# Kernel optimization log

Measured on AMD Instinct MI355X. Metric: run time of the kernel, lower is better.

## Reference

```python
import jax, jax.numpy as jnp
import numpy as np

UNITS = 1024
FT_DIM = 512
TIME_HORIZON = 512
INVERT_INDEX = 64
BATCH = 64


def setup_inputs() -> dict:
    key = jax.random.key(0)
    k1, k2, k3 = jax.random.split(key, 3)
    inputs = jax.random.normal(k1, (BATCH, TIME_HORIZON, FT_DIM), dtype=jnp.float32)
    # R ~ RandomNormal(stddev=1/time_horizon)
    R = jax.random.normal(k2, (FT_DIM, UNITS), dtype=jnp.float32) * (1.0 / TIME_HORIZON)
    # W ~ Orthogonal initializer
    A = jax.random.normal(k3, (UNITS, UNITS), dtype=jnp.float32)
    W, _ = jnp.linalg.qr(A)
    bias = jnp.zeros((UNITS,), dtype=jnp.float32)
    x0 = jnp.zeros((UNITS,), dtype=jnp.float32)
    return {"inputs": inputs, "R": R, "W": W, "bias": bias, "x0": x0}


def reference(inputs, R, W, bias, x0):
    B, T, _ = inputs.shape
    U = W.shape[0]
    W_inv = jnp.linalg.inv(W)
    # Precompute input projections for all steps: [T, B, U]
    h_all = jnp.einsum('btf,fu->tbu', inputs, R)
    # ct starts at 1, flips at every i % invert_index == 0 (including i=0),
    # so step i uses W iff (i // invert_index) is odd, else W_inv.
    use_W = ((jnp.arange(T) // INVERT_INDEX) % 2 == 1)
    state0 = jnp.broadcast_to(x0, (B, U))

    def step(state, xs):
        h, flag = xs
        Wt = jnp.where(flag, W, W_inv)
        new_state = jnp.tanh(h + state @ Wt + bias)
        return new_state, new_state

    _, states = jax.lax.scan(step, state0, (h_all, use_W))
    return states  # [T, B, U] == the list of per-step states
```

## Files before the change

kernel.cpp:

```cpp
#include <hip/hip_runtime.h>


#define TSTEPS 512

typedef __attribute__((ext_vector_type(4))) float f32x4;
typedef __attribute__((ext_vector_type(8))) _Float16 f16x8;
typedef unsigned long long u64;
typedef unsigned int u32;

union pk2 { _Float16 h[2]; u32 u; };

__device__ __forceinline__ f32x4 mfma16(f16x8 a, f16x8 b, f32x4 c){
  return __builtin_amdgcn_mfma_f32_16x16x32_f16(a, b, c, 0, 0, 0);
}
__device__ __forceinline__ f32x4 gload_sc1_b128(const void* p){
  f32x4 r;
  asm volatile("global_load_dwordx4 %0, %1, off sc1" : "=v"(r) : "v"(p) : "memory");
  return r;
}
__device__ __forceinline__ void gstore_sc1_b64(void* p, u64 d){
  asm volatile("global_store_dwordx2 %0, %1, off sc1" :: "v"(p), "v"(d) : "memory");
}
__device__ __forceinline__ void waitvm0(){
  asm volatile("s_waitcnt vmcnt(0)" ::: "memory");
}

__global__ void cvt_wr(const float* __restrict__ W, const float* __restrict__ R,
                       _Float16* __restrict__ Wa, _Float16* __restrict__ Wb,
                       _Float16* __restrict__ Rt){
  const int n  = gridDim.x * blockDim.x;
  const int id = blockIdx.x * blockDim.x + threadIdx.x;
  for (int i = id; i < 1024*1024; i += n){
    const float v = W[i];
    Wa[i] = (_Float16)v;
    const int k = i >> 10, u = i & 1023;
    Wb[u*1024 + k] = (_Float16)v;
  }
  for (int i = id; i < 512*1024; i += n){
    const int f = i >> 10, u = i & 1023;
    Rt[u*512 + f] = (_Float16)R[i];
  }
}

__global__ __launch_bounds__(512, 2) void h_prepass(
    const float* __restrict__ inputs, const _Float16* __restrict__ Rt,
    const float* __restrict__ bias, float* __restrict__ out){
  const int t  = blockIdx.x;
  const int w  = threadIdx.x >> 6, l = threadIdx.x & 63;
  const int lr = l & 15, lg = l >> 4;
  const int b0 = (w >> 1) * 16;
  const int c0 = (w & 1) * 512;

  f32x4 acc[32];
  #pragma unroll
  for (int n = 0; n < 32; ++n) acc[n] = (f32x4){0.f,0.f,0.f,0.f};

  for (int kc = 0; kc < 16; ++kc){
    const float* ip = inputs + (size_t)(b0 + lr)*262144 + (size_t)t*512 + kc*32 + lg*8;
    float4 xa = *(const float4*)ip, xb = *(const float4*)(ip + 4);
    f16x8 a;
    a[0]=(_Float16)xa.x; a[1]=(_Float16)xa.y; a[2]=(_Float16)xa.z; a[3]=(_Float16)xa.w;
    a[4]=(_Float16)xb.x; a[5]=(_Float16)xb.y; a[6]=(_Float16)xb.z; a[7]=(_Float16)xb.w;
    const _Float16* rp = Rt + (size_t)(c0 + lr)*512 + kc*32 + lg*8;
    #pragma unroll
    for (int n = 0; n < 32; ++n){
      f16x8 b = *(const f16x8*)(rp + (size_t)n*(16*512));
      acc[n] = mfma16(a, b, acc[n]);
    }
  }
  #pragma unroll
  for (int n = 0; n < 32; ++n){
    const int u = c0 + n*16 + lr;
    const float bu = bias[u];
    #pragma unroll
    for (int j = 0; j < 4; ++j)
      out[(size_t)t*65536 + (size_t)(b0 + lg*4 + j)*1024 + u] = acc[n][j] + bu;
  }
}

__global__ __launch_bounds__(512, 2) void irl_scan(
    const _Float16* __restrict__ Wa, const _Float16* __restrict__ Wb,
    const float* __restrict__ x0, float* __restrict__ out,
    unsigned short* __restrict__ st, unsigned* __restrict__ flags)
{
  __shared__ char alds[16 * 2048];

  const int tid = threadIdx.x;
  const int w   = tid >> 6;
  const int l   = tid & 63;
  const int lr  = l & 15;
  const int lg  = l >> 4;
  const int cblk = blockIdx.x & 7;
  const int grp  = blockIdx.x >> 3;
  const int col0 = cblk << 7;
  const int r0   = grp << 4;
  const int u    = col0 + w*16 + lr;
  unsigned* myf   = flags + (((grp << 3) + cblk) << 4);
  unsigned* pollf = flags + (((grp << 3) + w) << 4);

  {
    const int row = tid >> 5, cp = tid & 31;
    #pragma unroll
    for (int s = 0; s < 2; ++s){
      const int c = cp + s*32;
      pk2 p;
      p.h[0] = (_Float16)x0[col0 + 2*c];
      p.h[1] = (_Float16)x0[col0 + 2*c + 1];
      __hip_atomic_store((u32*)st + (size_t)(r0 + row)*512 + (col0 >> 1) + c, p.u,
                         __ATOMIC_RELAXED, __HIP_MEMORY_SCOPE_AGENT);
    }
  }
  __syncthreads();
  if (tid == 0)
    __hip_atomic_store(myf, 1u, __ATOMIC_RELAXED, __HIP_MEMORY_SCOPE_AGENT);

  unsigned cur = 0;
  int pp = -1;
  f16x8 wf[32];
  for (int t = 0; t < TSTEPS; ++t){
    const int ph = (t >> 6) & 1;
    if (ph != pp){
      pp = ph;
      const _Float16* Wsel = ph ? Wb : Wa;
      #pragma unroll
      for (int i = 0; i < 32; ++i)
        wf[i] = *(const f16x8*)(Wsel + (size_t)u*1024 + i*32 + lg*8);
    }

    float hv[4];
    #pragma unroll
    for (int j = 0; j < 4; ++j)
      hv[j] = out[(size_t)t*65536 + (size_t)(r0 + lg*4 + j)*1024 + u];

    if (w != cblk){
      const unsigned gen = (unsigned)(t + 1);
      for (;;){
        unsigned v = 0xffffffffu;
        if (l == 0)
          v = __hip_atomic_load(pollf, __ATOMIC_RELAXED, __HIP_MEMORY_SCOPE_AGENT);
        if (__all((int)(v >= gen))) break;
        __builtin_amdgcn_s_sleep(1);
      }
    }
    asm volatile("" ::: "memory");

    const char* stB = (const char*)st + ((size_t)cur << 17);
    f32x4 q[4];
    #pragma unroll
    for (int i = 0; i < 4; ++i){
      const int row = i*4 + lg;
      q[i] = gload_sc1_b128(stB + (size_t)(r0 + row)*2048 + w*256 + lr*16);
    }
    waitvm0();
    #pragma unroll
    for (int i = 0; i < 4; ++i){
      const int row = i*4 + lg;
      *(f32x4*)(alds + row*2048 + ((w*256 + lr*16) ^ ((row & 7) << 4))) = q[i];
    }
    __syncthreads();

    f32x4 ac0 = {0.f,0.f,0.f,0.f}, ac1 = ac0;
    #pragma unroll
    for (int i = 0; i < 32; i += 2){
      f16x8 a0 = *(const f16x8*)(alds + lr*2048 + ((i*64 + lg*16) ^ ((lr & 7) << 4)));
      f16x8 a1 = *(const f16x8*)(alds + lr*2048 + (((i+1)*64 + lg*16) ^ ((lr & 7) << 4)));
      ac0 = mfma16(a0, wf[i], ac0);
      ac1 = mfma16(a1, wf[i+1], ac1);
    }
    const f32x4 acc = ac0 + ac1;

    char* nbB = (char*)st + ((size_t)(cur ^ 1u) << 17);
    #pragma unroll
    for (int j = 0; j < 4; ++j){
      const int row = lg*4 + j;
      const float v = tanhf(acc[j] + hv[j]);
      __builtin_nontemporal_store(v, out + (size_t)t*65536 + (size_t)(r0 + row)*1024 + u);
      pk2 me; me.h[0] = (_Float16)v; me.h[1] = (_Float16)0.f;
      const u32 two = (me.u & 0xffffu) | ((u32)__shfl_xor((int)me.u, 1) << 16);
      const u64 four = (u64)two | ((u64)(u32)__shfl_xor((int)two, 2) << 32);
      if (!(lr & 3))
        gstore_sc1_b64(nbB + (size_t)(r0 + row)*2048 + (size_t)(u & ~3)*2, four);
    }

    cur ^= 1u;
    if (t < TSTEPS - 1){
      waitvm0();
      __syncthreads();
      if (tid == 0)
        __hip_atomic_store(myf, (unsigned)(t + 2), __ATOMIC_RELAXED, __HIP_MEMORY_SCOPE_AGENT);
    }
  }
}

extern "C" void kernel_launch(void* const* d_in, const int* in_sizes, int n_in,
                              void* d_out, int out_size, void* d_ws, size_t ws_size,
                              hipStream_t stream){
  (void)in_sizes; (void)n_in; (void)out_size; (void)ws_size;
  const float* inputs = (const float*)d_in[0];
  const float* R      = (const float*)d_in[1];
  const float* W      = (const float*)d_in[2];
  const float* bias   = (const float*)d_in[3];
  const float* x0     = (const float*)d_in[4];
  float* out = (float*)d_out;

  char* ws = (char*)d_ws;
  unsigned* flags     = (unsigned*)ws;
  unsigned short* st  = (unsigned short*)(ws + 4096);
  _Float16* Rt = (_Float16*)(ws + (512<<10));
  _Float16* Wa = (_Float16*)(ws + (2u<<20));
  _Float16* Wb = (_Float16*)(ws + (4u<<20));

  hipMemsetAsync(flags, 0, 4096, stream);
  hipLaunchKernelGGL(cvt_wr,    dim3(1024), dim3(256), 0, stream, W, R, Wa, Wb, Rt);
  hipLaunchKernelGGL(h_prepass, dim3(512),  dim3(512), 0, stream, inputs, Rt, bias, out);
  hipLaunchKernelGGL(irl_scan,  dim3(32),   dim3(512), 0, stream, Wa, Wb, x0, out, st, flags);
}
```

Baseline: 2.234 ms.

## Replace per-step flag handshake with parity tags embedded in state chunks

```diff
diff --git a/kernel.cpp b/kernel.cpp
--- a/kernel.cpp
+++ b/kernel.cpp
@@ -9,20 +9,17 @@
 typedef unsigned int u32;
 
 union pk2 { _Float16 h[2]; u32 u; };
+union chunk16 { f32x4 f; u32 d[4]; _Float16 h[8]; };
 
 __device__ __forceinline__ f32x4 mfma16(f16x8 a, f16x8 b, f32x4 c){
   return __builtin_amdgcn_mfma_f32_16x16x32_f16(a, b, c, 0, 0, 0);
 }
+__device__ __forceinline__ void waitvm0(){ asm volatile("s_waitcnt vmcnt(0)" ::: "memory"); }
 __device__ __forceinline__ f32x4 gload_sc1_b128(const void* p){
-  f32x4 r;
-  asm volatile("global_load_dwordx4 %0, %1, off sc1" : "=v"(r) : "v"(p) : "memory");
-  return r;
-}
-__device__ __forceinline__ void gstore_sc1_b64(void* p, u64 d){
-  asm volatile("global_store_dwordx2 %0, %1, off sc1" :: "v"(p), "v"(d) : "memory");
-}
-__device__ __forceinline__ void waitvm0(){
-  asm volatile("s_waitcnt vmcnt(0)" ::: "memory");
+  f32x4 r; asm volatile("global_load_dwordx4 %0, %1, off sc1" : "=v"(r) : "v"(p) : "memory"); return r;
+}
+__device__ __forceinline__ void gstore_sc1_b128(void* p, f32x4 d){
+  asm volatile("global_store_dwordx4 %0, %1, off sc1" :: "v"(p), "v"(d) : "memory");
 }
 
 __global__ void cvt_wr(const float* __restrict__ W, const float* __restrict__ R,
@@ -95,24 +92,30 @@
   const int col0 = cblk << 7;
   const int r0   = grp << 4;
   const int u    = col0 + w*16 + lr;
-  unsigned* myf   = flags + (((grp << 3) + cblk) << 4);
-  unsigned* pollf = flags + (((grp << 3) + w) << 4);
-
-  {
-    const int row = tid >> 5, cp = tid & 31;
-    #pragma unroll
-    for (int s = 0; s < 2; ++s){
-      const int c = cp + s*32;
-      pk2 p;
-      p.h[0] = (_Float16)x0[col0 + 2*c];
-      p.h[1] = (_Float16)x0[col0 + 2*c + 1];
-      __hip_atomic_store((u32*)st + (size_t)(r0 + row)*512 + (col0 >> 1) + c, p.u,
-                         __ATOMIC_RELAXED, __HIP_MEMORY_SCOPE_AGENT);
-    }
-  }
+  unsigned* myf  = flags + (((grp << 3) + cblk) << 4);
+
+  if (tid < 256){
+    const int row = tid >> 4, ch = tid & 15;
+    chunk16 c;
+    #pragma unroll
+    for (int j = 0; j < 8; ++j) c.h[j] = (_Float16)x0[col0 + ch*8 + j];
+    c.d[3] |= 0x10000u;
+    gstore_sc1_b128((char*)st + (size_t)(r0 + row)*2048 + col0*2 + ch*16, c.f);
+  }
+  waitvm0();
   __syncthreads();
   if (tid == 0)
     __hip_atomic_store(myf, 1u, __ATOMIC_RELAXED, __HIP_MEMORY_SCOPE_AGENT);
+  if (tid < 64){
+    const int src = (tid < 8) ? tid : 0;
+    const unsigned* pf = flags + (((grp << 3) + src) << 4);
+    for (;;){
+      unsigned v = __hip_atomic_load(pf, __ATOMIC_RELAXED, __HIP_MEMORY_SCOPE_AGENT);
+      if (__all((int)(v >= 1u))) break;
+      __builtin_amdgcn_s_sleep(1);
+    }
+  }
+  __syncthreads();
 
   unsigned cur = 0;
   int pp = -1;
@@ -132,30 +135,27 @@
     for (int j = 0; j < 4; ++j)
       hv[j] = out[(size_t)t*65536 + (size_t)(r0 + lg*4 + j)*1024 + u];
 
-    if (w != cblk){
-      const unsigned gen = (unsigned)(t + 1);
-      for (;;){
-        unsigned v = 0xffffffffu;
-        if (l == 0)
-          v = __hip_atomic_load(pollf, __ATOMIC_RELAXED, __HIP_MEMORY_SCOPE_AGENT);
-        if (__all((int)(v >= gen))) break;
-        __builtin_amdgcn_s_sleep(1);
-      }
-    }
-    asm volatile("" ::: "memory");
-
-    const char* stB = (const char*)st + ((size_t)cur << 17);
-    f32x4 q[4];
+    const u32 tag_exp = (((u32)t >> 1) & 1u) ^ 1u;
+    const char* base = (const char*)st + ((size_t)cur << 17)
+                     + (size_t)r0*2048 + w*256 + lr*16;
+    chunk16 q[4];
+    for (;;){
+      #pragma unroll
+      for (int i = 0; i < 4; ++i)
+        q[i].f = gload_sc1_b128(base + (size_t)(i*4 + lg)*2048);
+      waitvm0();
+      int ok = 1;
+      #pragma unroll
+      for (int i = 0; i < 4; ++i)
+        ok &= (int)(((q[i].d[3] >> 16) & 1u) == tag_exp);
+      if (__all(ok)) break;
+      __builtin_amdgcn_s_sleep(1);
+    }
+    __syncthreads();
     #pragma unroll
     for (int i = 0; i < 4; ++i){
-      const int row = i*4 + lg;
-      q[i] = gload_sc1_b128(stB + (size_t)(r0 + row)*2048 + w*256 + lr*16);
-    }
-    waitvm0();
-    #pragma unroll
-    for (int i = 0; i < 4; ++i){
-      const int row = i*4 + lg;
-      *(f32x4*)(alds + row*2048 + ((w*256 + lr*16) ^ ((row & 7) << 4))) = q[i];
+      const int row = i*4 + lg, c = w*256 + lr*16;
+      *(f32x4*)(alds + row*2048 + (c ^ ((row & 7) << 4))) = q[i].f;
     }
     __syncthreads();
 
@@ -170,25 +170,27 @@
     const f32x4 acc = ac0 + ac1;
 
     char* nbB = (char*)st + ((size_t)(cur ^ 1u) << 17);
+    const u32 tag_nxt = (((u32)(t + 1) >> 1) & 1u) ^ 1u;
     #pragma unroll
     for (int j = 0; j < 4; ++j){
       const int row = lg*4 + j;
       const float v = tanhf(acc[j] + hv[j]);
       __builtin_nontemporal_store(v, out + (size_t)t*65536 + (size_t)(r0 + row)*1024 + u);
       pk2 me; me.h[0] = (_Float16)v; me.h[1] = (_Float16)0.f;
-      const u32 two = (me.u & 0xffffu) | ((u32)__shfl_xor((int)me.u, 1) << 16);
-      const u64 four = (u64)two | ((u64)(u32)__shfl_xor((int)two, 2) << 32);
-      if (!(lr & 3))
-        gstore_sc1_b64(nbB + (size_t)(r0 + row)*2048 + (size_t)(u & ~3)*2, four);
+      const u32 two  = (me.u & 0xffffu) | ((u32)__shfl_xor((int)me.u, 1) << 16);
+      const u32 lo4  = two, hi4 = (u32)__shfl_xor((int)two, 2);
+      chunk16 cst;
+      cst.d[0] = (lr & 2) ? hi4 : lo4;
+      cst.d[1] = (lr & 2) ? lo4 : hi4;
+      cst.d[0] = lo4; cst.d[1] = hi4;
+      cst.d[2] = (u32)__shfl_xor((int)lo4, 4);
+      cst.d[3] = (u32)__shfl_xor((int)hi4, 4);
+      cst.d[3] = (cst.d[3] & ~0x10000u) | (tag_nxt << 16);
+      if (!(lr & 7))
+        gstore_sc1_b128(nbB + (size_t)(r0 + row)*2048 + (size_t)(u & ~7)*2, cst.f);
     }
 
     cur ^= 1u;
-    if (t < TSTEPS - 1){
-      waitvm0();
-      __syncthreads();
-      if (tid == 0)
-        __hip_atomic_store(myf, (unsigned)(t + 2), __ATOMIC_RELAXED, __HIP_MEMORY_SCOPE_AGENT);
-    }
   }
 }
 
```

Result: slower. 2.294 ms (+2.7%).
